# Kernel optimization log

Measured on AMD Instinct MI355X. Metric: run time of the kernel, lower is better.

Reference implementation:

```python
import jax, jax.numpy as jnp
import numpy as np

HQ, HK, DH = 32, 8, 64
ROPE_BASE = 10000.0


def _rope_tables(T, dtype):
    pos = jnp.arange(T, dtype=jnp.float32)
    inv_freq = 1.0 / (ROPE_BASE ** (jnp.arange(0, DH, 2, dtype=jnp.float32) / DH))
    freqs = pos[:, None] * inv_freq[None, :]          # (T, DH/2)
    cos = jnp.concatenate([jnp.cos(freqs), jnp.cos(freqs)], -1).astype(dtype)  # (T, DH)
    sin = jnp.concatenate([jnp.sin(freqs), jnp.sin(freqs)], -1).astype(dtype)
    return cos, sin


def _rotate_half(t):
    return jnp.concatenate([-t[..., DH // 2:], t[..., :DH // 2]], -1)


def setup_inputs() -> dict:
    key = jax.random.key(0)
    k1, k2, k3, k4 = jax.random.split(key, 4)
    B, T, D = 2, 2048, 2048
    std = 0.02 / np.sqrt(24)
    kv_std = std / np.sqrt(HQ / HK)
    return {
        "x": jax.random.normal(k1, (B, T, D), jnp.float32),
        "Wq": jax.random.normal(k2, (D, HQ * DH), jnp.float32) * std,
        "Wkv": jax.random.normal(k3, (D, 2 * HK * DH), jnp.float32) * kv_std,
        "Wo": jax.random.normal(k4, (HQ * DH, D), jnp.float32) * std,
    }


def reference(x, Wq, Wkv, Wo):
    B, T, D = x.shape
    g = HQ // HK
    scale = DH ** -0.5
    # projections
    q = (x @ Wq).reshape(B, T, HQ, DH).transpose(0, 2, 1, 3)       # (B,Hq,T,Dh)
    kv = (x @ Wkv).reshape(B, T, 2, HK, DH)
    k = kv[:, :, 0].transpose(0, 2, 1, 3)                           # (B,Hk,T,Dh)
    v = kv[:, :, 1].transpose(0, 2, 1, 3)
    # GQA expand: each kv head repeated g times consecutively
    k = jnp.repeat(k, g, axis=1)                                    # (B,Hq,T,Dh)
    v = jnp.repeat(v, g, axis=1)
    # RoPE on q and repeated k
    cos, sin = _rope_tables(T, x.dtype)
    q = q * cos + _rotate_half(q) * sin
    k = k * cos + _rotate_half(k) * sin
    # attention
    scores = jnp.einsum('bhqd,bhkd->bhqk', q, k) * scale            # (B,Hq,T,T)
    causal = jnp.triu(jnp.ones((T, T), bool), 1)
    scores = jnp.where(causal, -jnp.inf, scores)
    attn = jax.nn.softmax(scores.astype(jnp.float32), axis=-1).astype(x.dtype)
    out = jnp.einsum('bhqk,bhkd->bhqd', attn, v)                    # (B,Hq,T,Dh)
    out = out.transpose(0, 2, 1, 3).reshape(B, T, HQ * DH)
    return out @ Wo
```

## Files before the change

kernel.cpp:

```cpp
#include <hip/hip_runtime.h>
#include <hip/hip_bf16.h>

#define DEVI __device__ __forceinline__

typedef __attribute__((ext_vector_type(4))) float f32x4;
typedef __attribute__((ext_vector_type(16))) float f32x16;
typedef __attribute__((ext_vector_type(8))) short s16x8;
typedef __attribute__((ext_vector_type(4))) short s16x4;
typedef __attribute__((ext_vector_type(2))) unsigned u32x2;

DEVI ushort f2bf(float f) {
  union { float f; unsigned u; } v; v.f = f;
  unsigned r = v.u + 0x7FFFu + ((v.u >> 16) & 1u);
  return (ushort)(r >> 16);
}

DEVI void gload_lds16(const void* g, void* l) {
  __builtin_amdgcn_global_load_lds((const __attribute__((address_space(1))) void*)g,
                                   (__attribute__((address_space(3))) void*)l, 16, 0, 0);
}

#define MFMA16 __builtin_amdgcn_mfma_f32_16x16x32_bf16
#define SBAR() __builtin_amdgcn_s_barrier()
#define LGKM0() asm volatile("s_waitcnt lgkmcnt(0)")

DEVI float plswap_max(float x) {
  union { float f; unsigned u; } a; a.f = x;
  u32x2 r = __builtin_amdgcn_permlane32_swap(a.u, a.u, false, false);
  union { unsigned u; float f; } o0, o1; o0.u = r[0]; o1.u = r[1];
  return fmaxf(o0.f, o1.f);
}
DEVI float plswap_sum(float x) {
  union { float f; unsigned u; } a; a.f = x;
  u32x2 r = __builtin_amdgcn_permlane32_swap(a.u, a.u, false, false);
  union { unsigned u; float f; } o0, o1; o0.u = r[0]; o1.u = r[1];
  return o0.f + o1.f;
}

DEVI void stage128q(const ushort* __restrict__ gsrc, int K, ushort* ld, int tid) {
  #pragma unroll
  for (int j = 0; j < 4; ++j) {
    const int ci = j * 256 + tid;
    const int row = ci >> 3, c = ci & 7;
    gload_lds16(gsrc + (size_t)row * K + ((c ^ (row & 7)) << 3),
                ld + (size_t)(j * 256 + (tid & ~63)) * 8);
  }
}

DEVI s16x8 ldfrag(const ushort* tile, int row, int kc) {
  return *(const s16x8*)((const char*)tile + row * 128 + ((kc ^ (row & 7)) << 4));
}

DEVI void kloop3(const ushort* __restrict__ A, const ushort* __restrict__ BT,
                 ushort* Asm, ushort* Bsm, int m0, int n0, int K, int NKT,
                 f32x4 (&acc)[4][4], int tid, int wm, int wn, int g, int l15) {
  stage128q(A + (size_t)m0 * K, K, Asm, tid);
  stage128q(BT + (size_t)n0 * K, K, Bsm, tid);
  stage128q(BT + (size_t)n0 * K + 64, K, Bsm + 8192, tid);
  asm volatile("s_waitcnt vmcnt(4)");
  SBAR();

  int rd = 0;
  #pragma unroll 1
  for (int t = 0; t < NKT; ++t) {
    const ushort* Ah = Asm + (t & 1) * 8192;
    const ushort* Bh = Bsm + rd * 8192;
    s16x8 af[4][2], bfr[4][2];

    #pragma unroll
    for (int ks = 0; ks < 2; ++ks) {
      #pragma unroll
      for (int ni = 0; ni < 4; ++ni)
        bfr[ni][ks] = ldfrag(Bh, wn * 64 + ni * 16 + l15, ks * 4 + g);
      #pragma unroll
      for (int mi = 0; mi < 4; ++mi)
        af[mi][ks] = ldfrag(Ah, wm * 64 + mi * 16 + l15, ks * 4 + g);
    }
    if (t + 1 < NKT)
      stage128q(A + (size_t)m0 * K + (t + 1) * 64, K, Asm + ((t + 1) & 1) * 8192, tid);
    int wr = rd + 2; if (wr >= 3) wr -= 3;
    if (t + 2 < NKT)
      stage128q(BT + (size_t)n0 * K + (t + 2) * 64, K, Bsm + wr * 8192, tid);

    LGKM0();
    __builtin_amdgcn_sched_barrier(0);
    __builtin_amdgcn_s_setprio(1);
    #pragma unroll
    for (int mi = 0; mi < 4; ++mi)
      #pragma unroll
      for (int ni = 0; ni < 2; ++ni)
        #pragma unroll
        for (int ks = 0; ks < 2; ++ks)
          acc[mi][ni] = MFMA16(af[mi][ks], bfr[ni][ks], acc[mi][ni], 0, 0, 0);
    #pragma unroll
    for (int mi = 0; mi < 4; ++mi)
      #pragma unroll
      for (int ni = 0; ni < 2; ++ni)
        #pragma unroll
        for (int ks = 0; ks < 2; ++ks)
          acc[mi][2 + ni] = MFMA16(af[mi][ks], bfr[2 + ni][ks], acc[mi][2 + ni], 0, 0, 0);
    __builtin_amdgcn_s_setprio(0);

    if (t + 2 < NKT)      asm volatile("s_waitcnt vmcnt(4)");
    else if (t + 1 < NKT) asm volatile("s_waitcnt vmcnt(0)");
    SBAR();
    rd = (rd == 2) ? 0 : rd + 1;
  }
}

__global__ __launch_bounds__(256) void cast_bf16_k(const float* __restrict__ in,
                                                   ushort* __restrict__ out, int n) {
  int i = (blockIdx.x * 256 + threadIdx.x) * 4;
  if (i >= n) return;
  float4 v = *(const float4*)(in + i);
  ushort4 o;
  o.x = f2bf(v.x); o.y = f2bf(v.y); o.z = f2bf(v.z); o.w = f2bf(v.w);
  *(ushort4*)(out + i) = o;
}

__global__ __launch_bounds__(256) void transpose_cast_k(const float* __restrict__ in,
                                                        ushort* __restrict__ out, int R, int C) {
  __shared__ ushort tile[64][66];
  const int r0 = blockIdx.y * 64, c0 = blockIdx.x * 64;
  const int tid = threadIdx.x;
  #pragma unroll
  for (int j = 0; j < 16; ++j) {
    int idx = j * 256 + tid;
    int r = idx >> 6, c = idx & 63;
    tile[c][r] = f2bf(in[(size_t)(r0 + r) * C + c0 + c]);
  }
  __syncthreads();
  #pragma unroll
  for (int j = 0; j < 16; ++j) {
    int idx = j * 256 + tid;
    int c = idx >> 6, r = idx & 63;
    out[(size_t)(c0 + c) * R + r0 + r] = tile[c][r];
  }
}

__global__ __launch_bounds__(256) void rope_table_k(float2* __restrict__ tab) {
  int idx = blockIdx.x * 256 + threadIdx.x;
  int t = idx >> 5, i = idx & 31;
  float inv = expf(-(float)i * 0.28782313662425575f);
  float ang = (float)t * inv;
  tab[idx] = make_float2(cosf(ang), sinf(ang));
}

__global__ __launch_bounds__(256) void gemm_qkv_3b(const ushort* __restrict__ A,
                                                   const ushort* __restrict__ BT,
                                                   const float2* __restrict__ tab,
                                                   ushort* __restrict__ Qp,
                                                   ushort* __restrict__ Kp,
                                                   ushort* __restrict__ Vp) {
  constexpr int K = 2048, NKT = 32;
  __shared__ __attribute__((aligned(128))) ushort smem[40960];
  ushort* Asm = smem;
  ushort* Bsm = smem + 16384;
  ushort* Ot = smem;

  const int tid = threadIdx.x;
  const int ln = tid & 63, wv = tid >> 6;
  const int g = ln >> 4, l15 = ln & 15, l31 = ln & 31, hi = ln >> 5;
  const int wm = wv >> 1, wn = wv & 1;
  const int m0 = blockIdx.y * 128, n0 = blockIdx.x * 128;

  f32x4 acc[4][4];
  #pragma unroll
  for (int i = 0; i < 4; ++i)
    #pragma unroll
    for (int j = 0; j < 4; ++j) acc[i][j] = (f32x4){0.f, 0.f, 0.f, 0.f};

  kloop3(A, BT, Asm, Bsm, m0, n0, K, NKT, acc, tid, wm, wn, g, l15);

  __syncthreads();
  const int bq = m0 >> 11;
  const int tg0 = m0 & 2047;
  const int type = (n0 < 2048) ? 0 : (n0 < 2560 ? 1 : 2);

  #pragma unroll
  for (int mi = 0; mi < 4; ++mi)
    #pragma unroll
    for (int r = 0; r < 4; ++r) {
      const int tl = wm * 64 + mi * 16 + g * 4 + r;
      const int t = tg0 + tl;
      #pragma unroll
      for (int ni = 0; ni < 4; ++ni) {
        const int cl = wn * 64 + ni * 16 + l15;
        float val = acc[mi][ni][r];
        float outv;
        if (type < 2) {
          float pairv = acc[mi][ni ^ 2][r];
          float2 cs = tab[t * 32 + (ni & 1) * 16 + l15];
          outv = (ni & 2) ? (val * cs.x + pairv * cs.y) : (val * cs.x - pairv * cs.y);
          if (type == 0) outv *= 0.18033688011112042f;
        } else {
          outv = val;
        }
        Ot[tl * 132 + cl] = f2bf(outv);
      }
    }
  __syncthreads();

  #pragma unroll
  for (int it = 0; it < 8; ++it) {
    const int id = wv * 8 + it;
    const int hl = id >> 4, q4 = (id >> 2) & 3, fi = id & 3;
    const int tile = (tg0 >> 5) + q4;
    if (type < 2) {
      const ushort* srow = Ot + (q4 * 32 + l31) * 132 + hl * 64 + fi * 16 + hi * 8;
      union { s16x4 h[2]; s16x8 v; } u;
      u.h[0] = *(const s16x4*)srow;
      u.h[1] = *(const s16x4*)(srow + 4);
      ushort* dst;
      if (type == 0) {
        const int h = (n0 >> 6) + hl;
        dst = Qp + (((size_t)(bq * 32 + h) * 64 + tile) * 4 + fi) * 512 + ln * 8;
      } else {
        const int h = ((n0 - 2048) >> 6) + hl;
        dst = Kp + (((size_t)(bq * 8 + h) * 64 + tile) * 4 + fi) * 512 + ln * 8;
      }
      *(s16x8*)dst = u.v;
    } else {
      const int hk = ((n0 - 2560) >> 6) + hl;
      const int col = hl * 64 + (fi & 1) * 32 + l31;
      const int row0 = q4 * 32 + (fi >> 1) * 16 + hi * 8;
      ushort o[8];
      #pragma unroll
      for (int j = 0; j < 8; ++j) o[j] = Ot[(row0 + j) * 132 + col];
      ushort* dst = Vp + (((size_t)(bq * 8 + hk) * 64 + tile) * 4 + fi) * 512 + ln * 8;
      *(s16x8*)dst = *(const s16x8*)o;
    }
  }
}

__global__ __launch_bounds__(256) void gemm_bt_3b(const ushort* __restrict__ A,
                                                  const ushort* __restrict__ BT,
                                                  float* __restrict__ C, int M, int N, int K) {
  __shared__ __attribute__((aligned(128))) ushort smem[40960];
  ushort* Asm = smem;
  ushort* Bsm = smem + 16384;

  const int tid = threadIdx.x;
  const int ln = tid & 63, wv = tid >> 6;
  const int g = ln >> 4, l15 = ln & 15;
  const int wm = wv >> 1, wn = wv & 1;
  const int m0 = blockIdx.y * 128, n0 = blockIdx.x * 128;
  const int NKT = K / 64;

  f32x4 acc[4][4];
  #pragma unroll
  for (int i = 0; i < 4; ++i)
    #pragma unroll
    for (int j = 0; j < 4; ++j) acc[i][j] = (f32x4){0.f, 0.f, 0.f, 0.f};

  kloop3(A, BT, Asm, Bsm, m0, n0, K, NKT, acc, tid, wm, wn, g, l15);

  #pragma unroll
  for (int mi = 0; mi < 4; ++mi)
    #pragma unroll
    for (int r = 0; r < 4; ++r) {
      int row = m0 + wm * 64 + mi * 16 + g * 4 + r;
      float* crow = C + (size_t)row * N + n0 + wn * 64 + l15;
      #pragma unroll
      for (int ni = 0; ni < 4; ++ni) crow[ni * 16] = acc[mi][ni][r];
    }
}

__global__ __launch_bounds__(256) void attn_k(const ushort* __restrict__ Qp,
                                              const ushort* __restrict__ Kp,
                                              const ushort* __restrict__ Vp,
                                              ushort* __restrict__ O) {
  __shared__ ushort ep[4][32 * 64];
  const int tid = threadIdx.x, wv = tid >> 6, ln = tid & 63;
  const int l31 = ln & 31, hi = ln >> 5;

  const int f = blockIdx.x + gridDim.x * (blockIdx.y + 32 * blockIdx.z);
  const int xcd = f & 7, j = f >> 3;
  const int pr = xcd + 8 * (j & 1);
  const int b = pr >> 3, hk = pr & 7;
  const int s = j >> 1;
  const int hq = hk * 4 + (s & 3);
  const int qtile = 63 - ((s >> 2) * 4 + wv);
  const int qw = qtile * 32;
  const int nt = qtile + 1;

  const ushort* Qh    = Qp + ((size_t)(b * 32 + hq)) * (64 * 2048);
  const ushort* Kbase = Kp + ((size_t)(b * 8 + hk)) * (64 * 2048);
  const ushort* Vbase = Vp + ((size_t)(b * 8 + hk)) * (64 * 2048);
  ushort* lds = ep[wv];

  s16x8 qf[4];
  {
    const ushort* qp_ = Qh + (size_t)qtile * 2048 + ln * 8;
    #pragma unroll
    for (int ks = 0; ks < 4; ++ks) qf[ks] = *(const s16x8*)(qp_ + ks * 512);
  }

  f32x16 z16;
  #pragma unroll
  for (int r = 0; r < 16; ++r) z16[r] = 0.f;

  f32x16 oacc[2];
  #pragma unroll
  for (int dt = 0; dt < 2; ++dt)
    #pragma unroll
    for (int r = 0; r < 16; ++r) oacc[dt][r] = 0.f;
  float m = -1e30f, l = 0.f;

  const ushort* kp = Kbase + ln * 8;
  const ushort* vp = Vbase + ln * 8;

  s16x8 kf[4];
  #pragma unroll
  for (int ks = 0; ks < 4; ++ks) kf[ks] = *(const s16x8*)(kp + ks * 512);
  kp += 2048;

  s16x8 vc[4];
  union pfu { unsigned u[4]; s16x8 v; };
  pfu pf0, pf1;

  #pragma unroll 1
  for (int kt = 0; kt < nt; ++kt) {
    if (kt) {
      __builtin_amdgcn_s_setprio(1);
      oacc[0] = __builtin_amdgcn_mfma_f32_32x32x16_bf16(vc[0], pf0.v, oacc[0], 0, 0, 0);
      oacc[1] = __builtin_amdgcn_mfma_f32_32x32x16_bf16(vc[1], pf0.v, oacc[1], 0, 0, 0);
      oacc[0] = __builtin_amdgcn_mfma_f32_32x32x16_bf16(vc[2], pf1.v, oacc[0], 0, 0, 0);
      oacc[1] = __builtin_amdgcn_mfma_f32_32x32x16_bf16(vc[3], pf1.v, oacc[1], 0, 0, 0);
      __builtin_amdgcn_s_setprio(0);
    }
    #pragma unroll
    for (int fi2 = 0; fi2 < 4; ++fi2) vc[fi2] = *(const s16x8*)(vp + fi2 * 512);
    vp += 2048;

    __builtin_amdgcn_s_setprio(1);
    f32x16 sp = __builtin_amdgcn_mfma_f32_32x32x16_bf16(kf[0], qf[0], z16, 0, 0, 0);
    sp = __builtin_amdgcn_mfma_f32_32x32x16_bf16(kf[1], qf[1], sp, 0, 0, 0);
    sp = __builtin_amdgcn_mfma_f32_32x32x16_bf16(kf[2], qf[2], sp, 0, 0, 0);
    sp = __builtin_amdgcn_mfma_f32_32x32x16_bf16(kf[3], qf[3], sp, 0, 0, 0);
    __builtin_amdgcn_s_setprio(0);

    if (kt + 1 < nt) {
      #pragma unroll
      for (int ks = 0; ks < 4; ++ks) kf[ks] = *(const s16x8*)(kp + ks * 512);
      kp += 2048;
    }

    if (kt == qtile) {
      #pragma unroll
      for (int r = 0; r < 16; ++r) {
        int key = (r & 3) + 8 * (r >> 2) + 4 * hi;
        if (key > l31) sp[r] = -1e30f;
      }
    }

    float t0 = fmaxf(fmaxf(sp[0], sp[1]), sp[2]);
    float t1 = fmaxf(fmaxf(sp[3], sp[4]), sp[5]);
    float t2 = fmaxf(fmaxf(sp[6], sp[7]), sp[8]);
    float t3 = fmaxf(fmaxf(sp[9], sp[10]), sp[11]);
    float t4 = fmaxf(fmaxf(sp[12], sp[13]), sp[14]);
    float u0 = fmaxf(fmaxf(t0, t1), t2);
    float u1 = fmaxf(fmaxf(t3, t4), sp[15]);
    float pm = plswap_max(fmaxf(u0, u1));

    if (__any(pm - m > 8.0f)) {
      float mn = fmaxf(m, pm);
      float alpha = __builtin_amdgcn_exp2f(m - mn);
      m = mn;
      l *= alpha;
      #pragma unroll
      for (int dt = 0; dt < 2; ++dt)
        #pragma unroll
        for (int r = 0; r < 16; ++r) oacc[dt][r] *= alpha;
    }

    #pragma unroll
    for (int r = 0; r < 16; ++r) sp[r] = __builtin_amdgcn_exp2f(sp[r] - m);
    {
      float a0 = sp[0] + sp[1], a1 = sp[2] + sp[3], a2 = sp[4] + sp[5], a3 = sp[6] + sp[7];
      float a4 = sp[8] + sp[9], a5 = sp[10] + sp[11], a6 = sp[12] + sp[13], a7 = sp[14] + sp[15];
      float b0 = a0 + a1, b1 = a2 + a3, b2 = a4 + a5, b3 = a6 + a7;
      l += plswap_sum((b0 + b1) + (b2 + b3));
    }

    unsigned cw[8];
    #pragma unroll
    for (int jj = 0; jj < 8; ++jj) {
      union { __hip_bfloat162 h; unsigned u; } pk;
      pk.h = __float22bfloat162_rn(make_float2(sp[2 * jj], sp[2 * jj + 1]));
      cw[jj] = pk.u;
    }
    {
      u32x2 r;
      r = __builtin_amdgcn_permlane32_swap(cw[0], cw[2], false, false);
      pf0.u[0] = r[0]; pf0.u[2] = r[1];
      r = __builtin_amdgcn_permlane32_swap(cw[1], cw[3], false, false);
      pf0.u[1] = r[0]; pf0.u[3] = r[1];
      r = __builtin_amdgcn_permlane32_swap(cw[4], cw[6], false, false);
      pf1.u[0] = r[0]; pf1.u[2] = r[1];
      r = __builtin_amdgcn_permlane32_swap(cw[5], cw[7], false, false);
      pf1.u[1] = r[0]; pf1.u[3] = r[1];
    }
  }

  __builtin_amdgcn_s_setprio(1);
  oacc[0] = __builtin_amdgcn_mfma_f32_32x32x16_bf16(vc[0], pf0.v, oacc[0], 0, 0, 0);
  oacc[1] = __builtin_amdgcn_mfma_f32_32x32x16_bf16(vc[1], pf0.v, oacc[1], 0, 0, 0);
  oacc[0] = __builtin_amdgcn_mfma_f32_32x32x16_bf16(vc[2], pf1.v, oacc[0], 0, 0, 0);
  oacc[1] = __builtin_amdgcn_mfma_f32_32x32x16_bf16(vc[3], pf1.v, oacc[1], 0, 0, 0);
  __builtin_amdgcn_s_setprio(0);

  float invl = 1.0f / l;
  #pragma unroll
  for (int dt = 0; dt < 2; ++dt)
    #pragma unroll
    for (int r = 0; r < 16; ++r) {
      int d = dt * 32 + (r & 3) + 8 * (r >> 2) + 4 * hi;
      int byte = (l31 * 128 + d * 2) ^ ((l31 & 7) << 4);
      *(ushort*)((char*)lds + byte) = f2bf(oacc[dt][r] * invl);
    }
  const int qr = ln >> 1, half = ln & 1;
  #pragma unroll
  for (int jj = 0; jj < 4; ++jj) {
    int byte = (qr * 128 + half * 64 + jj * 16) ^ ((qr & 7) << 4);
    s16x8 vrow = *(const s16x8*)((const char*)lds + byte);
    *(s16x8*)(O + ((size_t)(b * 2048 + qw + qr)) * 2048 + hq * 64 + half * 32 + jj * 8) = vrow;
  }
}

extern "C" void kernel_launch(void* const* d_in, const int* in_sizes, int n_in,
                              void* d_out, int out_size, void* d_ws, size_t ws_size,
                              hipStream_t stream) {
  const float* x   = (const float*)d_in[0];
  const float* Wq  = (const float*)d_in[1];
  const float* Wkv = (const float*)d_in[2];
  const float* Wo  = (const float*)d_in[3];
  float* out = (float*)d_out;

  char* ws = (char*)d_ws;
  ushort* xb     = (ushort*)(ws);
  ushort* WqkvT  = (ushort*)(ws + 16777216);
  ushort* WoT    = (ushort*)(ws + 29360128);
  float2* tab    = (float2*)(ws + 37748736);
  ushort* Qp     = (ushort*)(ws + 38273024);
  ushort* Kp     = (ushort*)(ws + 55050240);
  ushort* Vp     = (ushort*)(ws + 59244544);
  ushort* Ob     = (ushort*)(ws + 63438848);

  cast_bf16_k<<<8192, 256, 0, stream>>>(x, xb, 2 * 2048 * 2048);
  transpose_cast_k<<<dim3(32, 32), 256, 0, stream>>>(Wq, WqkvT, 2048, 2048);
  transpose_cast_k<<<dim3(16, 32), 256, 0, stream>>>(Wkv, WqkvT + 2048 * 2048, 2048, 1024);
  transpose_cast_k<<<dim3(32, 32), 256, 0, stream>>>(Wo, WoT, 2048, 2048);
  rope_table_k<<<256, 256, 0, stream>>>(tab);
  gemm_qkv_3b<<<dim3(24, 32), 256, 0, stream>>>(xb, WqkvT, tab, Qp, Kp, Vp);
  attn_k<<<dim3(16, 32, 2), 256, 0, stream>>>(Qp, Kp, Vp, Ob);
  gemm_bt_3b<<<dim3(16, 32), 256, 0, stream>>>(Ob, WoT, out, 4096, 2048, 2048);
}
```

Baseline: 210.7 us.

## Replace output projection GEMM with 256x128 tile, K=32 steps, XCD-aware remap

```diff
diff --git a/kernel.cpp b/kernel.cpp
--- a/kernel.cpp
+++ b/kernel.cpp
@@ -46,9 +46,30 @@
                 ld + (size_t)(j * 256 + (tid & ~63)) * 8);
   }
 }
-
 DEVI s16x8 ldfrag(const ushort* tile, int row, int kc) {
   return *(const s16x8*)((const char*)tile + row * 128 + ((kc ^ (row & 7)) << 4));
+}
+
+DEVI void stageA32(const ushort* __restrict__ gsrc, int K, ushort* ld, int tid) {
+  #pragma unroll
+  for (int j = 0; j < 4; ++j) {
+    const int ci = j * 256 + tid;
+    const int row = ci >> 2, c = ci & 3;
+    gload_lds16(gsrc + (size_t)row * K + ((c ^ ((row >> 1) & 3)) << 3),
+                ld + (size_t)(j * 256 + (tid & ~63)) * 8);
+  }
+}
+DEVI void stageB32(const ushort* __restrict__ gsrc, int K, ushort* ld, int tid) {
+  #pragma unroll
+  for (int j = 0; j < 2; ++j) {
+    const int ci = j * 256 + tid;
+    const int row = ci >> 2, c = ci & 3;
+    gload_lds16(gsrc + (size_t)row * K + ((c ^ ((row >> 1) & 3)) << 3),
+                ld + (size_t)(j * 256 + (tid & ~63)) * 8);
+  }
+}
+DEVI s16x8 ldfrag32(const ushort* tile, int row, int g) {
+  return *(const s16x8*)((const char*)tile + row * 64 + ((g ^ ((row >> 1) & 3)) << 4));
 }
 
 DEVI void kloop3(const ushort* __restrict__ A, const ushort* __restrict__ BT,
@@ -233,10 +254,13 @@
   }
 }
 
-__global__ __launch_bounds__(256) void gemm_bt_3b(const ushort* __restrict__ A,
-                                                  const ushort* __restrict__ BT,
-                                                  float* __restrict__ C, int M, int N, int K) {
-  __shared__ __attribute__((aligned(128))) ushort smem[40960];
+__global__ __attribute__((amdgpu_flat_work_group_size(256, 256)))
+__attribute__((amdgpu_waves_per_eu(2, 2)))
+void gemm_wo_256(const ushort* __restrict__ A,
+                 const ushort* __restrict__ BT,
+                 float* __restrict__ C) {
+  constexpr int N = 2048, K = 2048, NKT = 64, GX = 16, NWG = 256;
+  __shared__ __attribute__((aligned(128))) ushort smem[28672];
   ushort* Asm = smem;
   ushort* Bsm = smem + 16384;
 
@@ -244,22 +268,65 @@
   const int ln = tid & 63, wv = tid >> 6;
   const int g = ln >> 4, l15 = ln & 15;
   const int wm = wv >> 1, wn = wv & 1;
-  const int m0 = blockIdx.y * 128, n0 = blockIdx.x * 128;
-  const int NKT = K / 64;
-
-  f32x4 acc[4][4];
-  #pragma unroll
-  for (int i = 0; i < 4; ++i)
+
+  const int orig = blockIdx.x;
+  const int wg = (orig & 7) * (NWG / 8) + (orig >> 3);
+  const int bx = wg % GX, by = wg / GX;
+  const int m0 = by * 256, n0 = bx * 128;
+
+  f32x4 acc[8][4];
+  #pragma unroll
+  for (int i = 0; i < 8; ++i)
     #pragma unroll
     for (int j = 0; j < 4; ++j) acc[i][j] = (f32x4){0.f, 0.f, 0.f, 0.f};
 
-  kloop3(A, BT, Asm, Bsm, m0, n0, K, NKT, acc, tid, wm, wn, g, l15);
-
-  #pragma unroll
-  for (int mi = 0; mi < 4; ++mi)
+  stageA32(A + (size_t)m0 * K, K, Asm, tid);
+  stageB32(BT + (size_t)n0 * K, K, Bsm, tid);
+  stageB32(BT + (size_t)n0 * K + 32, K, Bsm + 4096, tid);
+  asm volatile("s_waitcnt vmcnt(2)");
+  SBAR();
+
+  int rd = 0;
+  #pragma unroll 1
+  for (int t = 0; t < NKT; ++t) {
+    const ushort* Ah = Asm + (t & 1) * 8192;
+    const ushort* Bh = Bsm + rd * 4096;
+    s16x8 af[8], bfr[4];
+
+    #pragma unroll
+    for (int ni = 0; ni < 4; ++ni)
+      bfr[ni] = ldfrag32(Bh, wn * 64 + ni * 16 + l15, g);
+    #pragma unroll
+    for (int mi = 0; mi < 8; ++mi)
+      af[mi] = ldfrag32(Ah, wm * 128 + mi * 16 + l15, g);
+
+    if (t + 1 < NKT)
+      stageA32(A + (size_t)m0 * K + (t + 1) * 32, K, Asm + ((t + 1) & 1) * 8192, tid);
+    int wr = rd + 2; if (wr >= 3) wr -= 3;
+    if (t + 2 < NKT)
+      stageB32(BT + (size_t)n0 * K + (t + 2) * 32, K, Bsm + wr * 4096, tid);
+
+    LGKM0();
+    __builtin_amdgcn_sched_barrier(0);
+    __builtin_amdgcn_s_setprio(1);
+    #pragma unroll
+    for (int mi = 0; mi < 8; ++mi)
+      #pragma unroll
+      for (int ni = 0; ni < 4; ++ni)
+        acc[mi][ni] = MFMA16(af[mi], bfr[ni], acc[mi][ni], 0, 0, 0);
+    __builtin_amdgcn_s_setprio(0);
+
+    if (t + 2 < NKT)      asm volatile("s_waitcnt vmcnt(2)");
+    else if (t + 1 < NKT) asm volatile("s_waitcnt vmcnt(0)");
+    SBAR();
+    rd = (rd == 2) ? 0 : rd + 1;
+  }
+
+  #pragma unroll
+  for (int mi = 0; mi < 8; ++mi)
     #pragma unroll
     for (int r = 0; r < 4; ++r) {
-      int row = m0 + wm * 64 + mi * 16 + g * 4 + r;
+      int row = m0 + wm * 128 + mi * 16 + g * 4 + r;
       float* crow = C + (size_t)row * N + n0 + wn * 64 + l15;
       #pragma unroll
       for (int ni = 0; ni < 4; ++ni) crow[ni * 16] = acc[mi][ni][r];
@@ -454,5 +521,5 @@
   rope_table_k<<<256, 256, 0, stream>>>(tab);
   gemm_qkv_3b<<<dim3(24, 32), 256, 0, stream>>>(xb, WqkvT, tab, Qp, Kp, Vp);
   attn_k<<<dim3(16, 32, 2), 256, 0, stream>>>(Qp, Kp, Vp, Ob);
-  gemm_bt_3b<<<dim3(16, 32), 256, 0, stream>>>(Ob, WoT, out, 4096, 2048, 2048);
-}
+  gemm_wo_256<<<256, 256, 0, stream>>>(Ob, WoT, out);
+}
```

Measured after the change: 221.3 us. +5.0%, slower.
